# Performance work log

Measured on AMD Instinct MI355X. Metric: run time of the kernel, lower is better.

The kernel has to match this reference:

```python
import jax, jax.numpy as jnp
import numpy as np
import math

D_MODEL = 768
N_HEADS = 12
D_K = D_MODEL // N_HEADS
B, S = 2, 2048  # S == block_size


def setup_inputs() -> dict:
    key = jax.random.key(0)
    ks = jax.random.split(key, 5)
    scale = 1.0 / math.sqrt(D_MODEL)
    return {
        "x": jax.random.normal(ks[0], (B, S, D_MODEL), dtype=jnp.float32),
        "wq": jax.random.normal(ks[1], (D_MODEL, D_MODEL), dtype=jnp.float32) * scale,
        "bq": jnp.zeros((D_MODEL,), dtype=jnp.float32),
        "wk": jax.random.normal(ks[2], (D_MODEL, D_MODEL), dtype=jnp.float32) * scale,
        "bk": jnp.zeros((D_MODEL,), dtype=jnp.float32),
        "wv": jax.random.normal(ks[3], (D_MODEL, D_MODEL), dtype=jnp.float32) * scale,
        "bv": jnp.zeros((D_MODEL,), dtype=jnp.float32),
        "wo": jax.random.normal(ks[4], (D_MODEL, D_MODEL), dtype=jnp.float32) * scale,
        "bo": jnp.zeros((D_MODEL,), dtype=jnp.float32),
        "mask": 1,
    }


def reference(x, wq, bq, wk, bk, wv, bv, wo, bo, mask):
    b, s, _ = x.shape
    # projections (torch Linear: y = x @ W^T + b)
    q = (x @ wq.T + bq).reshape(b, s, N_HEADS, D_K).transpose(0, 2, 1, 3)  # bhsd
    k = (x @ wk.T + bk).reshape(b, s, N_HEADS, D_K).transpose(0, 2, 1, 3)
    v = (x @ wv.T + bv).reshape(b, s, N_HEADS, D_K).transpose(0, 2, 1, 3)
    scores = jnp.einsum("bhqd,bhkd->bhqk", q, k) / math.sqrt(D_K)  # [B,H,S,S]
    if mask:
        causal = jnp.tril(jnp.ones((s, s), dtype=bool))
        scores = jnp.where(causal, scores, -jnp.inf)
    attn = jax.nn.softmax(scores, axis=-1)
    # dropout = 0.0 (eval-mode): identity
    out = jnp.einsum("bhqk,bhkd->bhqd", attn, v)
    out = out.transpose(0, 2, 1, 3).reshape(b, s, D_MODEL)
    return out @ wo.T + bo
```

## Files before the change

### kernel.cpp

```cpp
#include <hip/hip_runtime.h>


#define DM   768
#define SEQ  2048
#define NB   2
#define NH   12
#define DK   64
#define MROWS (NB*SEQ)
#define QSCALE 0.18033688011112042f

typedef unsigned short u16;
typedef __bf16 bf16x8 __attribute__((ext_vector_type(8)));
typedef float  f32x4  __attribute__((ext_vector_type(4)));
typedef unsigned int u32x4 __attribute__((ext_vector_type(4)));

__device__ __forceinline__ u16 f2bf(float f) {
  unsigned u = __builtin_bit_cast(unsigned, f);
  u += 0x7fffu + ((u >> 16) & 1u);
  return (u16)(u >> 16);
}

__device__ __forceinline__ unsigned cvtpk(float lo, float hi) {
  unsigned r;
  asm("v_cvt_pk_bf16_f32 %0, %1, %2" : "=v"(r) : "v"(lo), "v"(hi));
  return r;
}

__device__ __forceinline__ bf16x8 ldbf8(const u16* p) {
  return __builtin_bit_cast(bf16x8, *(const u32x4*)p);
}

__device__ __forceinline__ void gl_lds16(const void* g, void* l) {
  __builtin_amdgcn_global_load_lds((__attribute__((address_space(1))) void*)g,
                                   (__attribute__((address_space(3))) void*)l,
                                   16, 0, 0);
}

__global__ void cvt_all(const float* __restrict__ x,
                        const float* __restrict__ w0, const float* __restrict__ w1,
                        const float* __restrict__ w2, const float* __restrict__ w3,
                        u16* __restrict__ dx, u16* __restrict__ dw,
                        int nx4, int nw4) {
  const int i = blockIdx.x * blockDim.x + threadIdx.x;
  const float* s; ushort4* d; int idx;
  if (i < nx4) {
    s = x; d = (ushort4*)dx; idx = i;
  } else {
    const int j = i - nx4;
    const int m = j / nw4;
    idx = j - m * nw4;
    s = (m == 0) ? w0 : (m == 1) ? w1 : (m == 2) ? w2 : w3;
    d = (ushort4*)dw + (size_t)m * nw4;
  }
  const float4 v = ((const float4*)s)[idx];
  ushort4 rr;
  rr.x = f2bf(v.x); rr.y = f2bf(v.y); rr.z = f2bf(v.z); rr.w = f2bf(v.w);
  d[idx] = rr;
}

template <int EPI, int TM>
__global__ __launch_bounds__(256, 3) void gemm_bt(
    const u16* __restrict__ A,
    const u16* __restrict__ B0, const u16* __restrict__ B1, const u16* __restrict__ B2,
    const float* __restrict__ bias0, const float* __restrict__ bias1, const float* __restrict__ bias2,
    u16* __restrict__ q_out, u16* __restrict__ k_out, u16* __restrict__ vt_out,
    float* __restrict__ f_out)
{
  constexpr int TN = 96;
  constexpr int MF = TM / 32;
  constexpr int NF = TN / 32;
  __shared__ u16 At[3][TM*32];
  __shared__ u16 Bt[3][TN*32];
  const int tid = threadIdx.x;
  const int w = tid >> 6, lane = tid & 63;
  const int lg = lane >> 4, ll = lane & 15;

  const int L = blockIdx.x;
  const int xcd = L & 7, li = L >> 3;
  int bm, bn;
  if (EPI == 0) { bm = xcd*4 + li/24; bn = li%24; }
  else          { bm = xcd*8 + li/8;  bn = li%8;  }
  const int row0 = bm * TM;

  const u16* Bm; const float* bias; int col0; int mat = 0;
  if (EPI == 0) {
    mat  = bn / 8;
    Bm   = (mat == 0) ? B0 : (mat == 1) ? B1 : B2;
    bias = (mat == 0) ? bias0 : (mat == 1) ? bias1 : bias2;
    col0 = (bn % 8) * TN;
  } else {
    Bm = B0; bias = bias0; col0 = bn * TN;
  }
  const int wr = w >> 1, wc = w & 1;

  f32x4 acc[MF][NF] = {};

#define GSTAGE(BUF, K0) do {                                                  \
    _Pragma("unroll")                                                         \
    for (int c = w; c < TM/16; c += 4) {                                      \
      const int a = c*1024 + lane*16;                                         \
      gl_lds16((const char*)A + ((size_t)(row0 + (a>>6))*DM + (K0))*2 + (a&63), \
               (char*)At[BUF] + c*1024);                                      \
    }                                                                         \
    _Pragma("unroll")                                                         \
    for (int c = w; c < TN/16; c += 4) {                                      \
      const int a = c*1024 + lane*16;                                         \
      gl_lds16((const char*)Bm + ((size_t)(col0 + (a>>6))*DM + (K0))*2 + (a&63), \
               (char*)Bt[BUF] + c*1024);                                      \
    }                                                                         \
  } while (0)

  GSTAGE(0, 0);
  GSTAGE(1, 32);
  int cur = 0;
  const int nsteps = DM / 32;
#pragma unroll 1
  for (int j = 0; j < nsteps; ++j) {
    if (j + 1 < nsteps) {
      if constexpr (TM == 128) asm volatile("s_waitcnt vmcnt(3)" ::: "memory");
      else                     asm volatile("s_waitcnt vmcnt(2)" ::: "memory");
    } else {
      asm volatile("s_waitcnt vmcnt(0)" ::: "memory");
    }
    __builtin_amdgcn_s_barrier();
    __builtin_amdgcn_sched_barrier(0);
    if (j + 2 < nsteps) {
      int nb = cur + 2; if (nb >= 3) nb -= 3;
      GSTAGE(nb, (j + 2) * 32);
    }

    bf16x8 fa[MF], fb[NF];
#pragma unroll
    for (int m = 0; m < MF; ++m)
      fa[m] = ldbf8(&At[cur][(wr*(TM/2) + m*16 + ll)*32 + lg*8]);
#pragma unroll
    for (int n = 0; n < NF; ++n)
      fb[n] = ldbf8(&Bt[cur][(wc*(TN/2) + n*16 + ll)*32 + lg*8]);
#pragma unroll
    for (int m = 0; m < MF; ++m)
#pragma unroll
      for (int n = 0; n < NF; ++n)
        acc[m][n] = __builtin_amdgcn_mfma_f32_16x16x32_bf16(fa[m], fb[n], acc[m][n], 0, 0, 0);
    cur = (cur == 2) ? 0 : cur + 1;
  }
#undef GSTAGE

#pragma unroll
  for (int m = 0; m < MF; ++m) {
#pragma unroll
    for (int n = 0; n < NF; ++n) {
      const int gn  = col0 + wc*(TN/2) + n*16 + ll;
      const float bv = bias[gn];
      const int gm0 = row0 + wr*(TM/2) + m*16 + lg*4;
#pragma unroll
      for (int j = 0; j < 4; ++j) {
        const float v = acc[m][n][j] + bv;
        const int gm = gm0 + j;
        if (EPI == 0) {
          const int b = gm >> 11, s = gm & 2047;
          const int h = gn >> 6,  d = gn & 63;
          const size_t bh = (size_t)(b*NH + h);
          if (mat == 0)      q_out[(bh*SEQ + s)*DK + d] = f2bf(v * QSCALE);
          else if (mat == 1) k_out[(bh*SEQ + s)*DK + d] = f2bf(v);
          else               vt_out[(bh*DK + d)*SEQ + s] = f2bf(v);
        } else {
          f_out[(size_t)gm*DM + gn] = v;
        }
      }
    }
  }
}

__device__ __forceinline__ void stage_kv(const u16* kp, const u16* vp, int kv0,
                                         u16* Kb, u16* Vb, int r, int lane) {
  const char* kg = (const char*)kp + (size_t)kv0 * 128;
  const char* vg = (const char*)vp + (size_t)kv0 * 2;
#pragma unroll
  for (int j = 0; j < 4; ++j) {
    const int base = (r*4 + j) * 1024;
    const int a = base + lane*16;
    const int row = a >> 7;
    const int cs  = ((a >> 4) & 7) ^ (row & 7);
    gl_lds16(kg + row*128 + cs*16, (char*)Kb + base);
    gl_lds16(vg + (size_t)row*4096 + cs*16, (char*)Vb + base);
  }
}

__device__ __forceinline__ bf16x8 ldtile(const u16* T, int row, int wo) {
  return ldbf8((const u16*)((const char*)T + row*128 + (wo ^ ((row & 7) << 4))));
}

__global__ __launch_bounds__(256, 3) void attn_fwd(
    const u16* __restrict__ qb, const u16* __restrict__ kb,
    const u16* __restrict__ vtb, u16* __restrict__ attb)
{
  __shared__ u16 KVb[2][2][64*64];
  __shared__ __align__(16) char arena[9216];
  const int L = blockIdx.x;
  const int xcd = L & 7, rr0 = L >> 3;
  const int bh = xcd * 3 + (rr0 % 3);
  const int pairb = rr0 / 3;
  const int tid = threadIdx.x;
  const int w = tid >> 6, lane = tid & 63;
  const int r = w & 1, h = w >> 1;
  const int lg = lane >> 4, ll = lane & 15;
  const u16* qp = qb  + (size_t)bh * SEQ * DK;
  const u16* kp = kb  + (size_t)bh * SEQ * DK;
  const u16* vp = vtb + (size_t)bh * DK * SEQ;
  const int b = bh / NH, hh = bh % NH;
  u16* Pl = (u16*)(arena + w*2304);
  float* mg = (float*)(arena + r*4608) + lane*18;

#pragma unroll 1
  for (int half = 0; half < 2; ++half) {
    const int tile = half ? pairb : 63 - pairb;
    const int nt = (tile >> 1) + 1;
    const int q0 = tile * 32 + r * 16;

    const bf16x8 qf0 = ldbf8(&qp[(size_t)(q0 + ll)*DK + lg*8]);
    const bf16x8 qf1 = ldbf8(&qp[(size_t)(q0 + ll)*DK + 32 + lg*8]);

    f32x4 o[4] = {};
    float mrun = 0.f, lrun = 0.f;

    const int nI = (nt + 1) >> 1;
    if (h < nt) stage_kv(kp, vp, h*64, KVb[h][0], KVb[h][1], r, lane);

#pragma unroll 1
    for (int i = 0; i < nI; ++i) {
      const int t = h + 2*i;
      asm volatile("s_waitcnt vmcnt(0)" ::: "memory");
      __builtin_amdgcn_s_barrier();
      __builtin_amdgcn_sched_barrier(0);

      if (t < nt) {
        const u16* Kc = KVb[h][0];
        const u16* Vc = KVb[h][1];

        f32x4 st[4] = {};
        __builtin_amdgcn_s_setprio(1);
#pragma unroll
        for (int kt = 0; kt < 4; ++kt) {
          const int rr = kt*16 + ll;
          st[kt] = __builtin_amdgcn_mfma_f32_16x16x32_bf16(ldtile(Kc, rr, lg*16),      qf0, st[kt], 0,0,0);
          st[kt] = __builtin_amdgcn_mfma_f32_16x16x32_bf16(ldtile(Kc, rr, 64 + lg*16), qf1, st[kt], 0,0,0);
        }
        __builtin_amdgcn_s_setprio(0);
        if (t == nt - 1) {
          const int kvb = t*64;
#pragma unroll
          for (int kt = 0; kt < 4; ++kt)
#pragma unroll
            for (int j = 0; j < 4; ++j)
              if (kvb + kt*16 + lg*4 + j > q0 + ll) st[kt][j] = -1e30f;
        }

        float lm = -1e30f;
#pragma unroll
        for (int kt = 0; kt < 4; ++kt)
          lm = fmaxf(lm, fmaxf(fmaxf(st[kt][0], st[kt][1]), fmaxf(st[kt][2], st[kt][3])));

        if (!__all(lm <= mrun + 8.f)) {
          float mt = lm;
          mt = fmaxf(mt, __shfl_xor(mt, 16));
          mt = fmaxf(mt, __shfl_xor(mt, 32));
          const float mn = fmaxf(mrun, mt);
          const float sc = exp2f(mrun - mn);
          lrun *= sc;
#pragma unroll
          for (int dt = 0; dt < 4; ++dt)
#pragma unroll
            for (int j = 0; j < 4; ++j)
              o[dt][j] *= sc;
          mrun = mn;
        }

        float psum = 0.f;
        unsigned pd[8];
#pragma unroll
        for (int kt = 0; kt < 4; ++kt) {
          const float e0 = exp2f(st[kt][0] - mrun);
          const float e1 = exp2f(st[kt][1] - mrun);
          const float e2 = exp2f(st[kt][2] - mrun);
          const float e3 = exp2f(st[kt][3] - mrun);
          psum += (e0 + e1) + (e2 + e3);
          pd[kt*2]   = cvtpk(e0, e1);
          pd[kt*2+1] = cvtpk(e2, e3);
        }
        lrun += psum;

#pragma unroll
        for (int kt = 0; kt < 4; ++kt)
          *(uint2*)&Pl[ll*72 + kt*16 + lg*4] = make_uint2(pd[kt*2], pd[kt*2+1]);
        const bf16x8 pb0 = ldbf8(&Pl[ll*72 + lg*8]);
        const bf16x8 pb1 = ldbf8(&Pl[ll*72 + 32 + lg*8]);

        __builtin_amdgcn_s_setprio(1);
#pragma unroll
        for (int dt = 0; dt < 4; ++dt) {
          const int rr = dt*16 + ll;
          o[dt] = __builtin_amdgcn_mfma_f32_16x16x32_bf16(ldtile(Vc, rr, lg*16),      pb0, o[dt], 0,0,0);
          o[dt] = __builtin_amdgcn_mfma_f32_16x16x32_bf16(ldtile(Vc, rr, 64 + lg*16), pb1, o[dt], 0,0,0);
        }
        __builtin_amdgcn_s_setprio(0);
      }

      __builtin_amdgcn_s_barrier();
      if (t + 2 < nt)
        stage_kv(kp, vp, (t+2)*64, KVb[h][0], KVb[h][1], r, lane);
    }

    float lt = lrun;
    lt += __shfl_xor(lt, 16);
    lt += __shfl_xor(lt, 32);

    __syncthreads();
    if (h == 1) {
#pragma unroll
      for (int dt = 0; dt < 4; ++dt)
#pragma unroll
        for (int j = 0; j < 4; ++j)
          mg[dt*4 + j] = o[dt][j];
      mg[16] = mrun;
      mg[17] = lt;
    }
    __syncthreads();
    if (h == 0) {
      const float mB = mg[16], lB = mg[17];
      const float ms = fmaxf(mrun, mB);
      const float sA = exp2f(mrun - ms), sB = exp2f(mB - ms);
      const float li = 1.0f / (lt * sA + lB * sB);
      u16* orow = &attb[(size_t)(b*SEQ + q0 + ll)*DM + hh*64];
#pragma unroll
      for (int dt = 0; dt < 4; ++dt) {
        ushort4 rw;
        rw.x = f2bf((o[dt][0]*sA + mg[dt*4+0]*sB) * li);
        rw.y = f2bf((o[dt][1]*sA + mg[dt*4+1]*sB) * li);
        rw.z = f2bf((o[dt][2]*sA + mg[dt*4+2]*sB) * li);
        rw.w = f2bf((o[dt][3]*sA + mg[dt*4+3]*sB) * li);
        *(ushort4*)&orow[dt*16 + lg*4] = rw;
      }
    }
    __syncthreads();
  }
}

extern "C" void kernel_launch(void* const* d_in, const int* in_sizes, int n_in,
                              void* d_out, int out_size, void* d_ws, size_t ws_size,
                              hipStream_t stream) {
  const float* x  = (const float*)d_in[0];
  const float* wq = (const float*)d_in[1];
  const float* bq = (const float*)d_in[2];
  const float* wk = (const float*)d_in[3];
  const float* bk = (const float*)d_in[4];
  const float* wv = (const float*)d_in[5];
  const float* bv = (const float*)d_in[6];
  const float* wo = (const float*)d_in[7];
  const float* bo = (const float*)d_in[8];
  float* out = (float*)d_out;

  char* ws = (char*)d_ws;
  u16* xb   = (u16*)(ws);
  u16* wqb  = (u16*)(ws + 6291456);
  u16* wkb  = (u16*)(ws + 7471104);
  u16* wvb  = (u16*)(ws + 8650752);
  u16* wob  = (u16*)(ws + 9830400);
  u16* qb   = (u16*)(ws + 11010048);
  u16* kb   = (u16*)(ws + 17301504);
  u16* vtb  = (u16*)(ws + 23592960);
  u16* attb = (u16*)(ws + 29884416);

  const int nx4 = MROWS*DM/4;
  const int nw4 = DM*DM/4;
  const int ntot = nx4 + 4*nw4;
  cvt_all<<<ntot/256, 256, 0, stream>>>(x, wq, wk, wv, wo, xb, wqb, nx4, nw4);

  gemm_bt<0,128><<<768, 256, 0, stream>>>(xb, wqb, wkb, wvb, bq, bk, bv,
                                          qb, kb, vtb, nullptr);
  attn_fwd<<<768, 256, 0, stream>>>(qb, kb, vtb, attb);
  gemm_bt<1,64><<<512, 256, 0, stream>>>(attb, wob, nullptr, nullptr, bo, nullptr, nullptr,
                                         nullptr, nullptr, nullptr, out);
}
```

Baseline: 93.25 us.

## Give each attention block one query tile and split KV columns across waves

Each attention block used to process a pair of query tiles (heavy plus light) and split KV tiles across two wave-pairs with double-buffered staging. Now each block handles one 32-row query tile, the grid doubles to 1536 blocks, and the four waves split each KV tile 2x2 (query half by KV half) using a single K/V LDS buffer. Partial softmax states are merged through shared memory in two steps. Launch bounds rise to 6 blocks per CU to raise occupancy, at the cost of losing double buffering, adding a barrier per KV tile, and depending on block scheduling order for load balance.

```diff
diff --git a/kernel.cpp b/kernel.cpp
--- a/kernel.cpp
+++ b/kernel.cpp
@@ -171,178 +171,180 @@
   }
 }
 
-__device__ __forceinline__ void stage_kv(const u16* kp, const u16* vp, int kv0,
-                                         u16* Kb, u16* Vb, int r, int lane) {
-  const char* kg = (const char*)kp + (size_t)kv0 * 128;
-  const char* vg = (const char*)vp + (size_t)kv0 * 2;
-#pragma unroll
-  for (int j = 0; j < 4; ++j) {
-    const int base = (r*4 + j) * 1024;
-    const int a = base + lane*16;
-    const int row = a >> 7;
-    const int cs  = ((a >> 4) & 7) ^ (row & 7);
-    gl_lds16(kg + row*128 + cs*16, (char*)Kb + base);
-    gl_lds16(vg + (size_t)row*4096 + cs*16, (char*)Vb + base);
-  }
-}
 
 __device__ __forceinline__ bf16x8 ldtile(const u16* T, int row, int wo) {
   return ldbf8((const u16*)((const char*)T + row*128 + (wo ^ ((row & 7) << 4))));
 }
 
-__global__ __launch_bounds__(256, 3) void attn_fwd(
+__global__ __launch_bounds__(256, 6) void attn_fwd(
     const u16* __restrict__ qb, const u16* __restrict__ kb,
     const u16* __restrict__ vtb, u16* __restrict__ attb)
 {
-  __shared__ u16 KVb[2][2][64*64];
+  __shared__ u16 Kt[64*64];
+  __shared__ u16 Vt[64*64];
   __shared__ __align__(16) char arena[9216];
   const int L = blockIdx.x;
-  const int xcd = L & 7, rr0 = L >> 3;
-  const int bh = xcd * 3 + (rr0 % 3);
-  const int pairb = rr0 / 3;
+  const int xcd = L & 7, li = L >> 3;
+  const int bh = xcd*3 + (li % 3);
+  const int tile = 63 - li/3;
   const int tid = threadIdx.x;
   const int w = tid >> 6, lane = tid & 63;
-  const int r = w & 1, h = w >> 1;
+  const int c = w & 1, r = w >> 1;
   const int lg = lane >> 4, ll = lane & 15;
   const u16* qp = qb  + (size_t)bh * SEQ * DK;
   const u16* kp = kb  + (size_t)bh * SEQ * DK;
   const u16* vp = vtb + (size_t)bh * DK * SEQ;
-  const int b = bh / NH, hh = bh % NH;
+  const int bb = bh / NH, hh = bh % NH;
+  const int nt = (tile >> 1) + 1;
+  const int q0 = tile*32 + c*16;
   u16* Pl = (u16*)(arena + w*2304);
-  float* mg = (float*)(arena + r*4608) + lane*18;
+  float* mg = (float*)(arena) + lane*18;
+
+  const bf16x8 qf0 = ldbf8(&qp[(size_t)(q0 + ll)*DK + lg*8]);
+  const bf16x8 qf1 = ldbf8(&qp[(size_t)(q0 + ll)*DK + 32 + lg*8]);
+
+  f32x4 o[4] = {};
+  float mrun = 0.f, lrun = 0.f;
+
+#define STAGE1(T) do {                                                        \
+    const char* kg_ = (const char*)kp + (size_t)(T) * 64 * 128;               \
+    const char* vg_ = (const char*)vp + (size_t)(T) * 128;                    \
+    _Pragma("unroll")                                                         \
+    for (int j2 = 0; j2 < 4; ++j2) {                                          \
+      if (w < 2) {                                                            \
+        const int base = (w*4 + j2) * 1024;                                   \
+        const int a = base + lane*16;                                         \
+        const int row = a >> 7;                                               \
+        const int cs = ((a >> 4) & 7) ^ (row & 7);                            \
+        gl_lds16(kg_ + row*128 + cs*16, (char*)Kt + base);                    \
+      } else {                                                                \
+        const int base = ((w-2)*4 + j2) * 1024;                               \
+        const int a = base + lane*16;                                         \
+        const int row = a >> 7;                                               \
+        const int cs = ((a >> 4) & 7) ^ (row & 7);                            \
+        gl_lds16(vg_ + (size_t)row*4096 + cs*16, (char*)Vt + base);           \
+      }                                                                       \
+    }                                                                         \
+  } while (0)
+
+  STAGE1(0);
 
 #pragma unroll 1
-  for (int half = 0; half < 2; ++half) {
-    const int tile = half ? pairb : 63 - pairb;
-    const int nt = (tile >> 1) + 1;
-    const int q0 = tile * 32 + r * 16;
-
-    const bf16x8 qf0 = ldbf8(&qp[(size_t)(q0 + ll)*DK + lg*8]);
-    const bf16x8 qf1 = ldbf8(&qp[(size_t)(q0 + ll)*DK + 32 + lg*8]);
-
-    f32x4 o[4] = {};
-    float mrun = 0.f, lrun = 0.f;
-
-    const int nI = (nt + 1) >> 1;
-    if (h < nt) stage_kv(kp, vp, h*64, KVb[h][0], KVb[h][1], r, lane);
-
-#pragma unroll 1
-    for (int i = 0; i < nI; ++i) {
-      const int t = h + 2*i;
-      asm volatile("s_waitcnt vmcnt(0)" ::: "memory");
-      __builtin_amdgcn_s_barrier();
-      __builtin_amdgcn_sched_barrier(0);
-
-      if (t < nt) {
-        const u16* Kc = KVb[h][0];
-        const u16* Vc = KVb[h][1];
-
-        f32x4 st[4] = {};
-        __builtin_amdgcn_s_setprio(1);
-#pragma unroll
-        for (int kt = 0; kt < 4; ++kt) {
-          const int rr = kt*16 + ll;
-          st[kt] = __builtin_amdgcn_mfma_f32_16x16x32_bf16(ldtile(Kc, rr, lg*16),      qf0, st[kt], 0,0,0);
-          st[kt] = __builtin_amdgcn_mfma_f32_16x16x32_bf16(ldtile(Kc, rr, 64 + lg*16), qf1, st[kt], 0,0,0);
-        }
-        __builtin_amdgcn_s_setprio(0);
-        if (t == nt - 1) {
-          const int kvb = t*64;
-#pragma unroll
-          for (int kt = 0; kt < 4; ++kt)
-#pragma unroll
-            for (int j = 0; j < 4; ++j)
-              if (kvb + kt*16 + lg*4 + j > q0 + ll) st[kt][j] = -1e30f;
-        }
-
-        float lm = -1e30f;
-#pragma unroll
-        for (int kt = 0; kt < 4; ++kt)
-          lm = fmaxf(lm, fmaxf(fmaxf(st[kt][0], st[kt][1]), fmaxf(st[kt][2], st[kt][3])));
-
-        if (!__all(lm <= mrun + 8.f)) {
-          float mt = lm;
-          mt = fmaxf(mt, __shfl_xor(mt, 16));
-          mt = fmaxf(mt, __shfl_xor(mt, 32));
-          const float mn = fmaxf(mrun, mt);
-          const float sc = exp2f(mrun - mn);
-          lrun *= sc;
-#pragma unroll
-          for (int dt = 0; dt < 4; ++dt)
-#pragma unroll
-            for (int j = 0; j < 4; ++j)
-              o[dt][j] *= sc;
-          mrun = mn;
-        }
-
-        float psum = 0.f;
-        unsigned pd[8];
-#pragma unroll
-        for (int kt = 0; kt < 4; ++kt) {
-          const float e0 = exp2f(st[kt][0] - mrun);
-          const float e1 = exp2f(st[kt][1] - mrun);
-          const float e2 = exp2f(st[kt][2] - mrun);
-          const float e3 = exp2f(st[kt][3] - mrun);
-          psum += (e0 + e1) + (e2 + e3);
-          pd[kt*2]   = cvtpk(e0, e1);
-          pd[kt*2+1] = cvtpk(e2, e3);
-        }
-        lrun += psum;
-
-#pragma unroll
-        for (int kt = 0; kt < 4; ++kt)
-          *(uint2*)&Pl[ll*72 + kt*16 + lg*4] = make_uint2(pd[kt*2], pd[kt*2+1]);
-        const bf16x8 pb0 = ldbf8(&Pl[ll*72 + lg*8]);
-        const bf16x8 pb1 = ldbf8(&Pl[ll*72 + 32 + lg*8]);
-
-        __builtin_amdgcn_s_setprio(1);
-#pragma unroll
-        for (int dt = 0; dt < 4; ++dt) {
-          const int rr = dt*16 + ll;
-          o[dt] = __builtin_amdgcn_mfma_f32_16x16x32_bf16(ldtile(Vc, rr, lg*16),      pb0, o[dt], 0,0,0);
-          o[dt] = __builtin_amdgcn_mfma_f32_16x16x32_bf16(ldtile(Vc, rr, 64 + lg*16), pb1, o[dt], 0,0,0);
-        }
-        __builtin_amdgcn_s_setprio(0);
-      }
-
-      __builtin_amdgcn_s_barrier();
-      if (t + 2 < nt)
-        stage_kv(kp, vp, (t+2)*64, KVb[h][0], KVb[h][1], r, lane);
-    }
-
-    float lt = lrun;
-    lt += __shfl_xor(lt, 16);
-    lt += __shfl_xor(lt, 32);
-
-    __syncthreads();
-    if (h == 1) {
+  for (int t = 0; t < nt; ++t) {
+    asm volatile("s_waitcnt vmcnt(0)" ::: "memory");
+    __builtin_amdgcn_s_barrier();
+    __builtin_amdgcn_sched_barrier(0);
+
+    f32x4 st[2] = {};
+    __builtin_amdgcn_s_setprio(1);
+#pragma unroll
+    for (int kt = 0; kt < 2; ++kt) {
+      const int row = r*32 + kt*16 + ll;
+      st[kt] = __builtin_amdgcn_mfma_f32_16x16x32_bf16(ldtile(Kt, row, lg*16),      qf0, st[kt], 0,0,0);
+      st[kt] = __builtin_amdgcn_mfma_f32_16x16x32_bf16(ldtile(Kt, row, 64 + lg*16), qf1, st[kt], 0,0,0);
+    }
+    __builtin_amdgcn_s_setprio(0);
+
+    if (t == nt - 1) {
+      const int kvb = t*64 + r*32;
+#pragma unroll
+      for (int kt = 0; kt < 2; ++kt)
+#pragma unroll
+        for (int j = 0; j < 4; ++j)
+          if (kvb + kt*16 + lg*4 + j > q0 + ll) st[kt][j] = -1e30f;
+    }
+
+    float lm = -1e30f;
+#pragma unroll
+    for (int kt = 0; kt < 2; ++kt)
+      lm = fmaxf(lm, fmaxf(fmaxf(st[kt][0], st[kt][1]), fmaxf(st[kt][2], st[kt][3])));
+
+    if (!__all(lm <= mrun + 8.f)) {
+      float mt = lm;
+      mt = fmaxf(mt, __shfl_xor(mt, 16));
+      mt = fmaxf(mt, __shfl_xor(mt, 32));
+      const float mn = fmaxf(mrun, mt);
+      const float sc = exp2f(mrun - mn);
+      lrun *= sc;
 #pragma unroll
       for (int dt = 0; dt < 4; ++dt)
 #pragma unroll
         for (int j = 0; j < 4; ++j)
-          mg[dt*4 + j] = o[dt][j];
-      mg[16] = mrun;
-      mg[17] = lt;
-    }
-    __syncthreads();
-    if (h == 0) {
-      const float mB = mg[16], lB = mg[17];
-      const float ms = fmaxf(mrun, mB);
-      const float sA = exp2f(mrun - ms), sB = exp2f(mB - ms);
-      const float li = 1.0f / (lt * sA + lB * sB);
-      u16* orow = &attb[(size_t)(b*SEQ + q0 + ll)*DM + hh*64];
-#pragma unroll
-      for (int dt = 0; dt < 4; ++dt) {
-        ushort4 rw;
-        rw.x = f2bf((o[dt][0]*sA + mg[dt*4+0]*sB) * li);
-        rw.y = f2bf((o[dt][1]*sA + mg[dt*4+1]*sB) * li);
-        rw.z = f2bf((o[dt][2]*sA + mg[dt*4+2]*sB) * li);
-        rw.w = f2bf((o[dt][3]*sA + mg[dt*4+3]*sB) * li);
-        *(ushort4*)&orow[dt*16 + lg*4] = rw;
-      }
-    }
-    __syncthreads();
-  }
+          o[dt][j] *= sc;
+      mrun = mn;
+    }
+
+    float psum = 0.f;
+    unsigned pd[4];
+#pragma unroll
+    for (int kt = 0; kt < 2; ++kt) {
+      const float e0 = exp2f(st[kt][0] - mrun);
+      const float e1 = exp2f(st[kt][1] - mrun);
+      const float e2 = exp2f(st[kt][2] - mrun);
+      const float e3 = exp2f(st[kt][3] - mrun);
+      psum += (e0 + e1) + (e2 + e3);
+      pd[kt*2]   = cvtpk(e0, e1);
+      pd[kt*2+1] = cvtpk(e2, e3);
+    }
+    lrun += psum;
+
+#pragma unroll
+    for (int kt = 0; kt < 2; ++kt)
+      *(uint2*)&Pl[ll*72 + kt*16 + lg*4] = make_uint2(pd[kt*2], pd[kt*2+1]);
+    const bf16x8 pb = ldbf8(&Pl[ll*72 + lg*8]);
+
+    __builtin_amdgcn_s_setprio(1);
+#pragma unroll
+    for (int dt = 0; dt < 4; ++dt)
+      o[dt] = __builtin_amdgcn_mfma_f32_16x16x32_bf16(
+                ldtile(Vt, dt*16 + ll, r*64 + lg*16), pb, o[dt], 0,0,0);
+    __builtin_amdgcn_s_setprio(0);
+
+    __builtin_amdgcn_s_barrier();
+    if (t + 1 < nt) STAGE1(t + 1);
+  }
+#undef STAGE1
+
+  float lt = lrun;
+  lt += __shfl_xor(lt, 16);
+  lt += __shfl_xor(lt, 32);
+
+#define PUBLISH() do {                                                   \
+    _Pragma("unroll")                                                    \
+    for (int dt = 0; dt < 4; ++dt)                                       \
+      _Pragma("unroll")                                                  \
+      for (int j = 0; j < 4; ++j)                                        \
+        mg[dt*4 + j] = o[dt][j];                                         \
+    mg[16] = mrun;                                                       \
+    mg[17] = lt;                                                         \
+  } while (0)
+#define MERGE_STORE() do {                                               \
+    const float mB = mg[16], lB = mg[17];                                \
+    const float ms = fmaxf(mrun, mB);                                    \
+    const float sA = exp2f(mrun - ms), sB = exp2f(mB - ms);              \
+    const float li2 = 1.0f / (lt * sA + lB * sB);                        \
+    u16* orow = &attb[(size_t)(bb*SEQ + q0 + ll)*DM + hh*64];            \
+    _Pragma("unroll")                                                    \
+    for (int dt = 0; dt < 4; ++dt) {                                     \
+      ushort4 rw;                                                        \
+      rw.x = f2bf((o[dt][0]*sA + mg[dt*4+0]*sB) * li2);                  \
+      rw.y = f2bf((o[dt][1]*sA + mg[dt*4+1]*sB) * li2);                  \
+      rw.z = f2bf((o[dt][2]*sA + mg[dt*4+2]*sB) * li2);                  \
+      rw.w = f2bf((o[dt][3]*sA + mg[dt*4+3]*sB) * li2);                  \
+      *(ushort4*)&orow[dt*16 + lg*4] = rw;                               \
+    }                                                                    \
+  } while (0)
+
+  __syncthreads();
+  if (w == 2) PUBLISH();
+  __syncthreads();
+  if (w == 0) MERGE_STORE();
+  __syncthreads();
+  if (w == 3) PUBLISH();
+  __syncthreads();
+  if (w == 1) MERGE_STORE();
+#undef PUBLISH
+#undef MERGE_STORE
 }
 
 extern "C" void kernel_launch(void* const* d_in, const int* in_sizes, int n_in,
@@ -377,7 +379,7 @@
 
   gemm_bt<0,128><<<768, 256, 0, stream>>>(xb, wqb, wkb, wvb, bq, bk, bv,
                                           qb, kb, vtb, nullptr);
-  attn_fwd<<<768, 256, 0, stream>>>(qb, kb, vtb, attb);
+  attn_fwd<<<1536, 256, 0, stream>>>(qb, kb, vtb, attb);
   gemm_bt<1,64><<<512, 256, 0, stream>>>(attb, wob, nullptr, nullptr, bo, nullptr, nullptr,
                                          nullptr, nullptr, nullptr, out);
 }
```

New measurement: 91.92 us (median of 2 runs). Within noise of the previous version (-1.4%).
